# Optimization experiments

Hardware: AMD Instinct MI355X
Metric: run time of the kernel (lower is better)

Reference implementation:

```python
import jax, jax.numpy as jnp
import numpy as np

B, M, D = 2048, 128, 5          # batch, max_atoms, max_degree
F_A, F_B, C = 62, 6, 128        # atom feats, bond feats, conv_width


def setup_inputs() -> dict:
    key = jax.random.key(0)
    k1, k2, k3, k4, k5 = jax.random.split(key, 5)
    atoms = jax.random.normal(k1, (B, M, F_A), dtype=jnp.float32)
    bonds = jax.random.uniform(k2, (B, M, D, F_B), dtype=jnp.float32)
    # edges in [-1, M-1]; -1 = no neighbour (padding)
    edges = jax.random.randint(k3, (B, M, D), 0, M + 1, dtype=jnp.int32) - 1
    fan = F_A + F_B
    scale = float(np.sqrt(2.0 / (fan + C)))
    W_inner = jax.random.normal(k4, (D, fan, C), dtype=jnp.float32) * scale
    b_inner = jnp.zeros((D, C), dtype=jnp.float32)
    W_self = jax.random.normal(k5, (fan, C), dtype=jnp.float32) * scale
    b_self = jnp.zeros((C,), dtype=jnp.float32)
    return {"atoms": atoms, "bonds": bonds, "edges": edges,
            "W_inner": W_inner, "b_inner": b_inner,
            "W_self": W_self, "b_self": b_self}


def reference(atoms, bonds, edges, W_inner, b_inner, W_self, b_self):
    # --- encode() of TiedGraphAutoencoder (encode_only=True) ---
    b = atoms.shape[0]
    # atom degree = number of non-(-1) entries per atom  (B, M)
    deg = jnp.sum((edges != -1).astype(jnp.float32), axis=-1)

    # neighbour_lookup: pad a zero atom at index 0, shift edges by +1,
    # batched gather -> (B, M, D, F_A)
    padded = jnp.pad(atoms, ((0, 0), (1, 0), (0, 0)))
    neigh = padded[jnp.arange(b)[:, None, None], edges + 1]

    summed_atoms = neigh.sum(axis=-2)          # (B, M, F_A)
    summed_bonds = bonds.sum(axis=-2)          # (B, M, F_B)
    summed_features = jnp.concatenate([summed_atoms, summed_bonds], axis=-1)

    # per-degree TimeDistributed Dense + relu, masked by (deg == d), summed
    h = jax.nn.relu(jnp.einsum('bmf,dfc->bmdc', summed_features, W_inner)
                    + b_inner)                 # (B, M, D, C)
    mask = (deg[..., None] == jnp.arange(D, dtype=jnp.float32)).astype(h.dtype)
    zni = jnp.einsum('bmdc,bmd->bmc', h, mask)  # (B, M, C)

    # self connection: dense on [atoms, summed_bonds]
    vxi = jnp.concatenate([atoms, summed_bonds], axis=-1)
    zxi = jax.nn.relu(vxi @ W_self + b_self)    # (B, M, C)

    return zni + zxi
```

## Files before the change

### kernel.cpp

```cpp
#include <hip/hip_runtime.h>

#define NB 2048
#define NM 128
#define ND 5
#define NFA 62
#define NFB 6
#define NFAN 68
#define NC 128
#define KTOT 96

typedef __bf16 bf16x8 __attribute__((ext_vector_type(8)));
typedef float floatx4 __attribute__((ext_vector_type(4)));

__device__ __forceinline__ unsigned short f2bf(float x) {
    unsigned u = __builtin_bit_cast(unsigned, x);
    u += 0x7FFFu + ((u >> 16) & 1u);
    return (unsigned short)(u >> 16);
}

__global__ __launch_bounds__(256) void prep_w(const float* __restrict__ W_self,
                                              unsigned short* __restrict__ wsb) {
    const int i = blockIdx.x * 256 + threadIdx.x;
    const int e     = i & 7;
    const int chunk = i >> 3;
    const int lane  = chunk & 63;
    const int cs    = chunk >> 6;
    const int ct    = cs / 3;
    const int slice = cs - 3 * ct;
    const int quad  = lane >> 4;
    const int col   = lane & 15;
    const int k     = slice * 32 + quad * 8 + e;
    const int c     = ct * 16 + col;
    unsigned short v = 0;
    if (k < NFAN) v = f2bf(W_self[k * NC + c]);
    wsb[i] = v;
}

__device__ __forceinline__ void glds16(const void* g, void* l) {
    __builtin_amdgcn_global_load_lds(
        (const __attribute__((address_space(1))) unsigned int*)g,
        (__attribute__((address_space(3))) unsigned int*)l,
        16, 0, 0);
}

__device__ __forceinline__ bf16x8 load8(const float* p) {
    float2 v0 = *(const float2*)(p);
    float2 v1 = *(const float2*)(p + 2);
    float2 v2 = *(const float2*)(p + 4);
    float2 v3 = *(const float2*)(p + 6);
    bf16x8 r;
    r[0] = (__bf16)v0.x; r[1] = (__bf16)v0.y; r[2] = (__bf16)v1.x; r[3] = (__bf16)v1.y;
    r[4] = (__bf16)v2.x; r[5] = (__bf16)v2.y; r[6] = (__bf16)v3.x; r[7] = (__bf16)v3.y;
    return r;
}

__device__ __forceinline__ bf16x8 load6bs(const float* p, const float* bs) {
    float2 v0 = *(const float2*)(p);
    float2 v1 = *(const float2*)(p + 2);
    float2 v2 = *(const float2*)(p + 4);
    float2 b01 = *(const float2*)(bs);
    bf16x8 r;
    r[0] = (__bf16)v0.x; r[1] = (__bf16)v0.y; r[2] = (__bf16)v1.x; r[3] = (__bf16)v1.y;
    r[4] = (__bf16)v2.x; r[5] = (__bf16)v2.y; r[6] = (__bf16)b01.x; r[7] = (__bf16)b01.y;
    return r;
}

__global__ __launch_bounds__(256) void tga_wave(
    const float* __restrict__ atoms,
    const float* __restrict__ bonds,
    const int*   __restrict__ edges,
    const float* __restrict__ W_inner,
    const float* __restrict__ b_inner,
    const float* __restrict__ b_self,
    const unsigned short* __restrict__ wsb,
    float* __restrict__ out)
{
    __shared__ __align__(16) unsigned short s_w[NC * KTOT];
    __shared__ __align__(16) float s_bsf[4][32][8];
    __shared__ float s_sf[4][64];

    const int tid  = threadIdx.x;
    const int w    = tid >> 6;
    const int lane = tid & 63;
    const int b    = blockIdx.x;
    const int m0   = w * 32;

    const float* atoms_b = atoms + (size_t)b * (NM * NFA);
    const float* bonds_b = bonds + (size_t)b * (NM * ND * NFB);
    const int*   edges_b = edges + (size_t)b * (NM * ND);
    float*       out_b   = out   + (size_t)b * (NM * NC);

    {
        const char* gw = (const char*)wsb;
        char* lw = (char*)s_w;
        for (int ch = w; ch < 24; ch += 4)
            glds16(gw + ch * 1024 + lane * 16, lw + ch * 1024);
    }

    int E0 = -1, E1 = -1, E2 = -1, E3 = -1, E4 = -1, deg = ND;
    if (lane < 32) {
        const int* e = edges_b + (m0 + lane) * ND;
        E0 = e[0]; E1 = e[1]; E2 = e[2]; E3 = e[3]; E4 = e[4];
        deg = (E0 >= 0) + (E1 >= 0) + (E2 >= 0) + (E3 >= 0) + (E4 >= 0);
    }
    unsigned long long smask = __ballot((lane < 32) && (deg < ND));

    {
        const int rb = lane >> 1, half = lane & 1;
        const float* bp = bonds_b + (m0 + rb) * (ND * NFB);
        float sb[NFB] = {0.f, 0.f, 0.f, 0.f, 0.f, 0.f};
        if (half == 0) {
            #pragma unroll
            for (int p = 0; p < 8; ++p) {
                float2 v = *(const float2*)&bp[2 * p];
                sb[(2 * p) % NFB]     += v.x;
                sb[(2 * p + 1) % NFB] += v.y;
            }
        } else {
            #pragma unroll
            for (int p = 8; p < 15; ++p) {
                float2 v = *(const float2*)&bp[2 * p];
                sb[(2 * p) % NFB]     += v.x;
                sb[(2 * p + 1) % NFB] += v.y;
            }
        }
        #pragma unroll
        for (int j = 0; j < NFB; ++j) sb[j] += __shfl_xor(sb[j], 1);
        if (half == 0) {
            *(float4*)&s_bsf[w][rb][0] = make_float4(sb[2], sb[3], sb[4], sb[5]);
            *(float2*)&s_bsf[w][rb][4] = make_float2(sb[0], sb[1]);
        }
    }

    const int col = lane & 15, quad = lane >> 4;
    const int lr0 = col, lr1 = 16 + col;
    const float* p0 = atoms_b + (m0 + lr0) * NFA;
    const float* p1 = atoms_b + (m0 + lr1) * NFA;

    bf16x8 a00 = load8(p0 + quad * 8);
    bf16x8 a10 = load8(p1 + quad * 8);

    __syncthreads();

    bf16x8 a01, a11;
    if (quad < 3) {
        a01 = load8(p0 + 32 + quad * 8);
        a11 = load8(p1 + 32 + quad * 8);
    } else {
        a01 = load6bs(p0 + 56, &s_bsf[w][lr0][4]);
        a11 = load6bs(p1 + 56, &s_bsf[w][lr1][4]);
    }
    bf16x8 a02, a12;
    #pragma unroll
    for (int j = 0; j < 8; ++j) { a02[j] = (__bf16)0.f; a12[j] = (__bf16)0.f; }
    if (quad == 0) {
        float4 q0 = *(const float4*)&s_bsf[w][lr0][0];
        float4 q1 = *(const float4*)&s_bsf[w][lr1][0];
        a02[0] = (__bf16)q0.x; a02[1] = (__bf16)q0.y; a02[2] = (__bf16)q0.z; a02[3] = (__bf16)q0.w;
        a12[0] = (__bf16)q1.x; a12[1] = (__bf16)q1.y; a12[2] = (__bf16)q1.z; a12[3] = (__bf16)q1.w;
    }

    floatx4 acc[16];
    #pragma unroll
    for (int t = 0; t < 16; ++t) { floatx4 z; z[0] = z[1] = z[2] = z[3] = 0.f; acc[t] = z; }

    const unsigned short* wl = s_w + lane * 8;
    #pragma unroll
    for (int ct = 0; ct < 8; ++ct) {
        bf16x8 wf0 = *(const bf16x8*)(wl + (ct * 3 + 0) * 512);
        bf16x8 wf1 = *(const bf16x8*)(wl + (ct * 3 + 1) * 512);
        bf16x8 wf2 = *(const bf16x8*)(wl + (ct * 3 + 2) * 512);
        acc[ct]     = __builtin_amdgcn_mfma_f32_16x16x32_bf16(a00, wf0, acc[ct],     0, 0, 0);
        acc[8 + ct] = __builtin_amdgcn_mfma_f32_16x16x32_bf16(a10, wf0, acc[8 + ct], 0, 0, 0);
        acc[ct]     = __builtin_amdgcn_mfma_f32_16x16x32_bf16(a01, wf1, acc[ct],     0, 0, 0);
        acc[8 + ct] = __builtin_amdgcn_mfma_f32_16x16x32_bf16(a11, wf1, acc[8 + ct], 0, 0, 0);
        acc[ct]     = __builtin_amdgcn_mfma_f32_16x16x32_bf16(a02, wf2, acc[ct],     0, 0, 0);
        acc[8 + ct] = __builtin_amdgcn_mfma_f32_16x16x32_bf16(a12, wf2, acc[8 + ct], 0, 0, 0);
    }

    #pragma unroll
    for (int ct = 0; ct < 8; ++ct) {
        const float bias = b_self[ct * 16 + col];
        #pragma unroll
        for (int rr = 0; rr < 4; ++rr) {
            const int row0 = m0 + quad * 4 + rr;
            out_b[row0 * NC + ct * 16 + col]        = fmaxf(acc[ct][rr]     + bias, 0.f);
            out_b[(row0 + 16) * NC + ct * 16 + col] = fmaxf(acc[8 + ct][rr] + bias, 0.f);
        }
    }

    while (smask) {
        const int ml = __ffsll(smask) - 1;
        smask &= smask - 1;
        const int m  = m0 + ml;
        const int d  = __shfl(deg, ml);
        const int e0 = __shfl(E0, ml), e1 = __shfl(E1, ml), e2 = __shfl(E2, ml),
                  e3 = __shfl(E3, ml), e4 = __shfl(E4, ml);

        if (lane < NFA) {
            float sv = 0.f;
            if (e0 >= 0) sv += atoms_b[e0 * NFA + lane];
            if (e1 >= 0) sv += atoms_b[e1 * NFA + lane];
            if (e2 >= 0) sv += atoms_b[e2 * NFA + lane];
            if (e3 >= 0) sv += atoms_b[e3 * NFA + lane];
            if (e4 >= 0) sv += atoms_b[e4 * NFA + lane];
            s_sf[w][lane] = sv;
        }
        __builtin_amdgcn_wave_barrier();

        const int c0 = 2 * lane;
        float2 bi = *(const float2*)&b_inner[d * NC + c0];
        float acc0 = bi.x, acc1 = bi.y;
        const float* Wd = W_inner + (size_t)d * (NFAN * NC);
        #pragma unroll
        for (int f = 0; f < NFA; ++f) {
            const float sfv = s_sf[w][f];
            float2 wv = *(const float2*)&Wd[f * NC + c0];
            acc0 += sfv * wv.x; acc1 += sfv * wv.y;
        }
        {
            const float* bb = &s_bsf[w][ml][0];
            const float fv[6] = {bb[4], bb[5], bb[0], bb[1], bb[2], bb[3]};
            #pragma unroll
            for (int j = 0; j < NFB; ++j) {
                float2 wv = *(const float2*)&Wd[(NFA + j) * NC + c0];
                acc0 += fv[j] * wv.x; acc1 += fv[j] * wv.y;
            }
        }
        float2 cur = *(float2*)&out_b[m * NC + c0];
        cur.x += fmaxf(acc0, 0.f);
        cur.y += fmaxf(acc1, 0.f);
        *(float2*)&out_b[m * NC + c0] = cur;
        __builtin_amdgcn_wave_barrier();
    }
}

extern "C" void kernel_launch(void* const* d_in, const int* in_sizes, int n_in,
                              void* d_out, int out_size, void* d_ws, size_t ws_size,
                              hipStream_t stream) {
    const float* atoms   = (const float*)d_in[0];
    const float* bonds   = (const float*)d_in[1];
    const int*   edges   = (const int*)d_in[2];
    const float* W_inner = (const float*)d_in[3];
    const float* b_inner = (const float*)d_in[4];
    const float* W_self  = (const float*)d_in[5];
    const float* b_self  = (const float*)d_in[6];
    float* out = (float*)d_out;
    unsigned short* wsb = (unsigned short*)d_ws;

    prep_w<<<(NC * KTOT) / 256, 256, 0, stream>>>(W_self, wsb);
    tga_wave<<<NB, 256, 0, stream>>>(atoms, bonds, edges, W_inner, b_inner,
                                     b_self, wsb, out);
}
```

Before: 257.3 us.

## Split batch blocks into single-wave blocks and stream weights from global

```diff
diff --git a/kernel.cpp b/kernel.cpp
--- a/kernel.cpp
+++ b/kernel.cpp
@@ -42,6 +42,12 @@
         (__attribute__((address_space(3))) unsigned int*)l,
         16, 0, 0);
 }
+__device__ __forceinline__ void glds4(const void* g, void* l) {
+    __builtin_amdgcn_global_load_lds(
+        (const __attribute__((address_space(1))) unsigned int*)g,
+        (__attribute__((address_space(3))) unsigned int*)l,
+        4, 0, 0);
+}
 
 __device__ __forceinline__ bf16x8 load8(const float* p) {
     float2 v0 = *(const float2*)(p);
@@ -65,7 +71,7 @@
     return r;
 }
 
-__global__ __launch_bounds__(256) void tga_wave(
+__global__ __launch_bounds__(64, 3) void tga_wave64(
     const float* __restrict__ atoms,
     const float* __restrict__ bonds,
     const int*   __restrict__ edges,
@@ -75,26 +81,27 @@
     const unsigned short* __restrict__ wsb,
     float* __restrict__ out)
 {
-    __shared__ __align__(16) unsigned short s_w[NC * KTOT];
-    __shared__ __align__(16) float s_bsf[4][32][8];
-    __shared__ float s_sf[4][64];
-
-    const int tid  = threadIdx.x;
-    const int w    = tid >> 6;
-    const int lane = tid & 63;
-    const int b    = blockIdx.x;
-    const int m0   = w * 32;
+    __shared__ __align__(16) float s_bonds[NM / 4 * ND * NFB];
+    __shared__ __align__(16) float s_bsf[32][8];
+    __shared__ float s_sf[64];
+
+    const int lane = threadIdx.x;
+    const int b    = blockIdx.x >> 2;
+    const int m0   = (blockIdx.x & 3) * 32;
 
     const float* atoms_b = atoms + (size_t)b * (NM * NFA);
-    const float* bonds_b = bonds + (size_t)b * (NM * ND * NFB);
     const int*   edges_b = edges + (size_t)b * (NM * ND);
     float*       out_b   = out   + (size_t)b * (NM * NC);
 
     {
-        const char* gw = (const char*)wsb;
-        char* lw = (char*)s_w;
-        for (int ch = w; ch < 24; ch += 4)
-            glds16(gw + ch * 1024 + lane * 16, lw + ch * 1024);
+        const char* gb = (const char*)bonds + ((size_t)b * NM + m0) * (ND * NFB * 4);
+        char* lb = (char*)s_bonds;
+        glds16(gb + 0 * 1024 + lane * 16, lb + 0 * 1024);
+        glds16(gb + 1 * 1024 + lane * 16, lb + 1 * 1024);
+        glds16(gb + 2 * 1024 + lane * 16, lb + 2 * 1024);
+        glds4(gb + 3072 + lane * 4, lb + 3072);
+        glds4(gb + 3328 + lane * 4, lb + 3328);
+        glds4(gb + 3584 + lane * 4, lb + 3584);
     }
 
     int E0 = -1, E1 = -1, E2 = -1, E3 = -1, E4 = -1, deg = ND;
@@ -105,9 +112,19 @@
     }
     unsigned long long smask = __ballot((lane < 32) && (deg < ND));
 
+    const int col = lane & 15, quad = lane >> 4;
+    const int lr0 = col, lr1 = 16 + col;
+    const float* p0 = atoms_b + (m0 + lr0) * NFA;
+    const float* p1 = atoms_b + (m0 + lr1) * NFA;
+    bf16x8 a00 = load8(p0 + quad * 8);
+    bf16x8 a10 = load8(p1 + quad * 8);
+
+    asm volatile("s_waitcnt vmcnt(0)" ::: "memory");
+    __builtin_amdgcn_wave_barrier();
+
     {
         const int rb = lane >> 1, half = lane & 1;
-        const float* bp = bonds_b + (m0 + rb) * (ND * NFB);
+        const float* bp = s_bonds + rb * (ND * NFB);
         float sb[NFB] = {0.f, 0.f, 0.f, 0.f, 0.f, 0.f};
         if (half == 0) {
             #pragma unroll
@@ -127,35 +144,26 @@
         #pragma unroll
         for (int j = 0; j < NFB; ++j) sb[j] += __shfl_xor(sb[j], 1);
         if (half == 0) {
-            *(float4*)&s_bsf[w][rb][0] = make_float4(sb[2], sb[3], sb[4], sb[5]);
-            *(float2*)&s_bsf[w][rb][4] = make_float2(sb[0], sb[1]);
-        }
-    }
-
-    const int col = lane & 15, quad = lane >> 4;
-    const int lr0 = col, lr1 = 16 + col;
-    const float* p0 = atoms_b + (m0 + lr0) * NFA;
-    const float* p1 = atoms_b + (m0 + lr1) * NFA;
-
-    bf16x8 a00 = load8(p0 + quad * 8);
-    bf16x8 a10 = load8(p1 + quad * 8);
-
-    __syncthreads();
+            *(float4*)&s_bsf[rb][0] = make_float4(sb[2], sb[3], sb[4], sb[5]);
+            *(float2*)&s_bsf[rb][4] = make_float2(sb[0], sb[1]);
+        }
+    }
+    __builtin_amdgcn_wave_barrier();
 
     bf16x8 a01, a11;
     if (quad < 3) {
         a01 = load8(p0 + 32 + quad * 8);
         a11 = load8(p1 + 32 + quad * 8);
     } else {
-        a01 = load6bs(p0 + 56, &s_bsf[w][lr0][4]);
-        a11 = load6bs(p1 + 56, &s_bsf[w][lr1][4]);
+        a01 = load6bs(p0 + 56, &s_bsf[lr0][4]);
+        a11 = load6bs(p1 + 56, &s_bsf[lr1][4]);
     }
     bf16x8 a02, a12;
     #pragma unroll
     for (int j = 0; j < 8; ++j) { a02[j] = (__bf16)0.f; a12[j] = (__bf16)0.f; }
     if (quad == 0) {
-        float4 q0 = *(const float4*)&s_bsf[w][lr0][0];
-        float4 q1 = *(const float4*)&s_bsf[w][lr1][0];
+        float4 q0 = *(const float4*)&s_bsf[lr0][0];
+        float4 q1 = *(const float4*)&s_bsf[lr1][0];
         a02[0] = (__bf16)q0.x; a02[1] = (__bf16)q0.y; a02[2] = (__bf16)q0.z; a02[3] = (__bf16)q0.w;
         a12[0] = (__bf16)q1.x; a12[1] = (__bf16)q1.y; a12[2] = (__bf16)q1.z; a12[3] = (__bf16)q1.w;
     }
@@ -164,12 +172,12 @@
     #pragma unroll
     for (int t = 0; t < 16; ++t) { floatx4 z; z[0] = z[1] = z[2] = z[3] = 0.f; acc[t] = z; }
 
-    const unsigned short* wl = s_w + lane * 8;
-    #pragma unroll
+    const unsigned short* wg = wsb + lane * 8;
+    #pragma unroll 2
     for (int ct = 0; ct < 8; ++ct) {
-        bf16x8 wf0 = *(const bf16x8*)(wl + (ct * 3 + 0) * 512);
-        bf16x8 wf1 = *(const bf16x8*)(wl + (ct * 3 + 1) * 512);
-        bf16x8 wf2 = *(const bf16x8*)(wl + (ct * 3 + 2) * 512);
+        bf16x8 wf0 = *(const bf16x8*)(wg + (ct * 3 + 0) * 512);
+        bf16x8 wf1 = *(const bf16x8*)(wg + (ct * 3 + 1) * 512);
+        bf16x8 wf2 = *(const bf16x8*)(wg + (ct * 3 + 2) * 512);
         acc[ct]     = __builtin_amdgcn_mfma_f32_16x16x32_bf16(a00, wf0, acc[ct],     0, 0, 0);
         acc[8 + ct] = __builtin_amdgcn_mfma_f32_16x16x32_bf16(a10, wf0, acc[8 + ct], 0, 0, 0);
         acc[ct]     = __builtin_amdgcn_mfma_f32_16x16x32_bf16(a01, wf1, acc[ct],     0, 0, 0);
@@ -204,7 +212,7 @@
             if (e2 >= 0) sv += atoms_b[e2 * NFA + lane];
             if (e3 >= 0) sv += atoms_b[e3 * NFA + lane];
             if (e4 >= 0) sv += atoms_b[e4 * NFA + lane];
-            s_sf[w][lane] = sv;
+            s_sf[lane] = sv;
         }
         __builtin_amdgcn_wave_barrier();
 
@@ -214,12 +222,12 @@
         const float* Wd = W_inner + (size_t)d * (NFAN * NC);
         #pragma unroll
         for (int f = 0; f < NFA; ++f) {
-            const float sfv = s_sf[w][f];
+            const float sfv = s_sf[f];
             float2 wv = *(const float2*)&Wd[f * NC + c0];
             acc0 += sfv * wv.x; acc1 += sfv * wv.y;
         }
         {
-            const float* bb = &s_bsf[w][ml][0];
+            const float* bb = &s_bsf[ml][0];
             const float fv[6] = {bb[4], bb[5], bb[0], bb[1], bb[2], bb[3]};
             #pragma unroll
             for (int j = 0; j < NFB; ++j) {
@@ -249,6 +257,6 @@
     unsigned short* wsb = (unsigned short*)d_ws;
 
     prep_w<<<(NC * KTOT) / 256, 256, 0, stream>>>(W_self, wsb);
-    tga_wave<<<NB, 256, 0, stream>>>(atoms, bonds, edges, W_inner, b_inner,
-                                     b_self, wsb, out);
-}
+    tga_wave64<<<NB * 4, 64, 0, stream>>>(atoms, bonds, edges, W_inner, b_inner,
+                                          b_self, wsb, out);
+}
```

Result: slower. 349.3 us (+35.8%).
